# Kernel tuning notes

Measured on AMD Instinct MI355X. Metric: run time of the kernel, lower is better.

The kernel has to match this reference:

```python
import jax, jax.numpy as jnp
import numpy as np

HEIGHT = 8
IN_DIM = 128
OUT_DIM = 8
BATCH = 65536
INT_NODES = 2 ** HEIGHT - 1   # 255
LEAF_NODES = 2 ** HEIGHT      # 256


def _and_weight(height):
    # Fixed +-1 structured routing matrix [leaf, int_nodes] (DGTreg._get_and_layer_params).
    leaf = 2 ** height
    w = np.zeros((leaf, leaf - 1), dtype=np.float32)
    for i in range(height):
        num = 2 ** i
        start = num - 1
        for j in range(start, start + num):
            rb = leaf // num * (j - start)
            rm = rb + leaf // (2 * num)
            re = rb + leaf // num
            w[rb:rm, j] = 1.0
            w[rm:re, j] = -1.0
    return jnp.asarray(w)


def setup_inputs() -> dict:
    key = jax.random.key(0)
    k = jax.random.split(key, 5)
    x = jax.random.normal(k[0], (BATCH, IN_DIM), jnp.float32)
    # orthogonal-ish predicate weight (scaled gaussian), zero bias per module init
    Wp = jax.random.normal(k[1], (INT_NODES, IN_DIM), jnp.float32) / np.sqrt(IN_DIM)
    bp = jnp.zeros((INT_NODES,), jnp.float32)
    Wand = _and_weight(HEIGHT)
    # xavier_uniform for or-layer weights [out_dim, in_dim, leaf]
    lim = np.sqrt(6.0 / (IN_DIM + LEAF_NODES)).astype(np.float32)
    Wor = jax.random.uniform(k[2], (OUT_DIM, IN_DIM, LEAF_NODES), jnp.float32, -lim, lim)
    bor = jax.random.normal(k[3], (OUT_DIM, IN_DIM), jnp.float32) * 0.01
    lim2 = np.sqrt(6.0 / (LEAF_NODES + OUT_DIM)).astype(np.float32)
    action_stds = jax.random.uniform(k[4], (LEAF_NODES, OUT_DIM), jnp.float32, -lim2, lim2)
    return {"x": x, "Wp": Wp, "bp": bp, "Wand": Wand, "Wor": Wor, "bor": bor,
            "action_stds": action_stds}


def reference(x, Wp, bp, Wand, Wor, bor, action_stds):
    sg = jax.lax.stop_gradient
    # predicate layer: [B, int_nodes]
    pred_z = x @ Wp.T + bp
    # ScaleBinarizer1: fac = mean(|z|) per row; binarize to {fac, 0}; straight-through grad
    fac = jnp.mean(jnp.abs(pred_z), axis=-1, keepdims=True)
    binz = jnp.where(pred_z >= 0, fac, 0.0)
    pred_a = pred_z + sg(binz - pred_z)          # forward = binz, grad = identity
    pred_a = 2.0 * pred_a - sg(fac)              # in {+fac, -fac}
    # fixed structured 'and' layer -> softmax over leaves
    and_z = pred_a @ Wand.T                      # [B, leaf]
    and_a = jax.nn.softmax(and_z, axis=-1)
    # Sparser1: keep only max entry per row, straight-through grad
    mx = jnp.max(and_a, axis=-1, keepdims=True)
    sp = jnp.where(and_a >= mx, and_a, 0.0)
    and_a = and_a + sg(sp - and_a)
    # or layers: per-output Linear(leaf->in_dim) then <wt, x>
    wt = jnp.einsum('bl,oil->boi', and_a, Wor) + bor[None]   # [B, out, in]
    out = jnp.einsum('boi,bi->bo', wt, x)                    # [B, out]
    # std head over detached routing weights
    std = jnp.sum(action_stds[None] * sg(and_a)[:, :, None], axis=1)  # [B, out]
    std = jnp.clip(std, -20.0, 2.0)
    return (out, std)
```

## Files before the change

kernel.cpp:

```cpp
#include <hip/hip_runtime.h>

#define BATCH 65536
#define IN_DIM 128
#define INT_NODES 255
#define LEAF 256
#define OUT_DIM 8
#define ROWS_PB 32
#define NBLK (BATCH / ROWS_PB)
#define AMB_TH 4e-3f

typedef float    f4v __attribute__((ext_vector_type(4)));
typedef _Float16 h8v __attribute__((ext_vector_type(8)));

__global__ __launch_bounds__(256) void prep(const float* __restrict__ Wor,
                                            float* __restrict__ Wor_t,
                                            const float* __restrict__ Wp,
                                            _Float16* __restrict__ Bf) {
    if (blockIdx.x < 64) {
        __shared__ float t[64][65];
        const int rt = blockIdx.x >> 2, ct = blockIdx.x & 3;
        const int r0 = rt * 64, c0 = ct * 64;
        const int tx = threadIdx.x & 63, ty = threadIdx.x >> 6;
#pragma unroll
        for (int p = 0; p < 16; ++p) {
            int r = ty + p * 4;
            t[r][tx] = Wor[(size_t)(r0 + r) * 256 + c0 + tx];
        }
        __syncthreads();
#pragma unroll
        for (int p = 0; p < 16; ++p) {
            int r = ty + p * 4;
            Wor_t[(size_t)(c0 + r) * 1024 + r0 + tx] = t[tx][r];
        }
    } else {
        int slot = (blockIdx.x - 64) * 256 + threadIdx.x;
        int j    = slot & 7;
        int lane = (slot >> 3) & 63;
        int ntg  = (slot >> 9) & 15;
        int ks   = slot >> 13;
        int n = ntg * 16 + (lane & 15);
        int k = ks * 32 + (lane >> 4) * 8 + j;
        float v = (n < INT_NODES) ? Wp[n * IN_DIM + k] : 0.f;
        Bf[slot] = (_Float16)v;
    }
}

__global__ __launch_bounds__(256) void dgt_main(
    const float* __restrict__ x, const float* __restrict__ Wp,
    const float* __restrict__ bp, const _Float16* __restrict__ Bfg,
    const float* __restrict__ Wor_t, const float* __restrict__ bor,
    const float* __restrict__ stds,
    float* __restrict__ out, float* __restrict__ stdo) {

    __shared__ unsigned char sgn[LEAF * 8];
    __shared__ float P[64 * 36];
    __shared__ float S[8 * 32];
    __shared__ float H[32 * 68];
    __shared__ float psL[32];
    __shared__ int   leafL[32];

    const int tid  = threadIdx.x;
    const int wave = tid >> 6;
    const int lane = tid & 63;
    const int c = lane & 15;
    const int g = lane >> 4;
    const int rowbase = blockIdx.x * ROWS_PB;

    f4v acc[2][4];
#pragma unroll
    for (int mt = 0; mt < 2; ++mt)
#pragma unroll
        for (int nt = 0; nt < 4; ++nt) acc[mt][nt] = (f4v){0.f, 0.f, 0.f, 0.f};

    const h8v* Bf8 = (const h8v*)Bfg;
    const float* xbase = x + (size_t)rowbase * IN_DIM;
#pragma unroll
    for (int ks = 0; ks < 4; ++ks) {
        h8v ah[2];
#pragma unroll
        for (int mt = 0; mt < 2; ++mt) {
            const float* p = xbase + (size_t)(mt * 16 + c) * IN_DIM + ks * 32 + g * 8;
            float4 v0 = *reinterpret_cast<const float4*>(p);
            float4 v1 = *reinterpret_cast<const float4*>(p + 4);
            h8v a;
            a[0] = (_Float16)v0.x; a[1] = (_Float16)v0.y;
            a[2] = (_Float16)v0.z; a[3] = (_Float16)v0.w;
            a[4] = (_Float16)v1.x; a[5] = (_Float16)v1.y;
            a[6] = (_Float16)v1.z; a[7] = (_Float16)v1.w;
            ah[mt] = a;
        }
#pragma unroll
        for (int nt = 0; nt < 4; ++nt) {
            h8v b = Bf8[(ks * 16 + (wave * 4 + nt)) * 64 + lane];
#pragma unroll
            for (int mt = 0; mt < 2; ++mt)
                acc[mt][nt] = __builtin_amdgcn_mfma_f32_16x16x32_f16(ah[mt], b, acc[mt][nt], 0, 0, 0);
        }
    }

    {
        float pp[2][4];
#pragma unroll
        for (int mt = 0; mt < 2; ++mt)
#pragma unroll
            for (int rr = 0; rr < 4; ++rr) pp[mt][rr] = 0.f;
#pragma unroll
        for (int nt = 0; nt < 4; ++nt) {
            const int n = wave * 64 + nt * 16 + c;
            const float bpv = (n < INT_NODES) ? bp[n] : 0.f;
#pragma unroll
            for (int mt = 0; mt < 2; ++mt) {
                unsigned by = 0;
#pragma unroll
                for (int rr = 0; rr < 4; ++rr) {
                    float v = acc[mt][nt][rr] + bpv;
                    float av = fabsf(v);
                    if (n < INT_NODES) pp[mt][rr] += av;
                    by |= ((v < 0.f ? 1u : 0u) | (av < AMB_TH ? 2u : 0u)) << (2 * rr);
                }
                sgn[n * 8 + mt * 4 + g] = (unsigned char)by;
            }
        }
#pragma unroll
        for (int mt = 0; mt < 2; ++mt)
#pragma unroll
            for (int rr = 0; rr < 4; ++rr)
                P[(wave * 16 + c) * 36 + mt * 16 + g * 4 + rr] = pp[mt][rr];
    }
    __syncthreads();

    {
        const int r = tid & 31, q = tid >> 5;
        float s = 0.f;
#pragma unroll
        for (int cc = 0; cc < 8; ++cc) s += P[(q * 8 + cc) * 36 + r];
        S[q * 32 + r] = s;
    }
    __syncthreads();

    {
        const int r = tid >> 3, kq = tid & 7;
        float asum = 0.f;
#pragma unroll
        for (int j = 0; j < 8; ++j) asum += S[j * 32 + r];
        const float fac = asum * (1.0f / (float)INT_NODES);
        const float e = expf(-2.0f * fac);
        const float qq = 1.0f + e;
        const float q2 = qq * qq, q4 = q2 * q2, q8 = q4 * q4;
        const float ps = 1.0f / q8;

        int node = 0;
#pragma unroll
        for (int d = 0; d < 8; ++d) {
            unsigned by = sgn[node * 8 + (r >> 2)];
            int code = (int)((by >> ((r & 3) * 2)) & 3u);
            int neg;
            if (code & 2) {
                double zd = (double)bp[node];
                const float* wr = Wp + node * IN_DIM;
                const float* xrow = x + (size_t)(rowbase + r) * IN_DIM;
                for (int k = 0; k < IN_DIM; ++k)
                    zd = fma((double)wr[k], (double)xrow[k], zd);
                neg = (zd < 0.0) ? 1 : 0;
            } else {
                neg = code & 1;
            }
            node = 2 * node + 1 + neg;
        }
        const int leaf = node - INT_NODES;
        if (kq == 0) { psL[r] = ps; leafL[r] = leaf; }

        const float* xr = x + (size_t)(rowbase + r) * IN_DIM;
        const float* wl = Wor_t + (size_t)leaf * 1024;
        float hp[8], tp[8];
#pragma unroll
        for (int o = 0; o < 8; ++o) { hp[o] = 0.f; tp[o] = 0.f; }
#pragma unroll
        for (int step = 0; step < 4; ++step) {
            const int off = (step * 8 + kq) * 4;
            float4 xv = *reinterpret_cast<const float4*>(xr + off);
#pragma unroll
            for (int o = 0; o < 8; ++o) {
                float4 wv = *reinterpret_cast<const float4*>(wl + o * IN_DIM + off);
                float4 bv = *reinterpret_cast<const float4*>(bor + o * IN_DIM + off);
                hp[o] = fmaf(wv.x, xv.x, hp[o]); hp[o] = fmaf(wv.y, xv.y, hp[o]);
                hp[o] = fmaf(wv.z, xv.z, hp[o]); hp[o] = fmaf(wv.w, xv.w, hp[o]);
                tp[o] = fmaf(bv.x, xv.x, tp[o]); tp[o] = fmaf(bv.y, xv.y, tp[o]);
                tp[o] = fmaf(bv.z, xv.z, tp[o]); tp[o] = fmaf(bv.w, xv.w, tp[o]);
            }
        }
#pragma unroll
        for (int o = 0; o < 8; ++o)
            H[r * 68 + o * 8 + kq] = ps * hp[o] + tp[o];
    }
    __syncthreads();

    {
        const int r = tid & 31, o = tid >> 5;
        const float* h = &H[r * 68 + o * 8];
        float v = ((h[0] + h[1]) + (h[2] + h[3])) + ((h[4] + h[5]) + (h[6] + h[7]));
        out[(size_t)(rowbase + r) * OUT_DIM + o] = v;
        float sd = psL[r] * stds[leafL[r] * OUT_DIM + o];
        stdo[(size_t)(rowbase + r) * OUT_DIM + o] = fminf(fmaxf(sd, -20.0f), 2.0f);
    }
}

extern "C" void kernel_launch(void* const* d_in, const int* in_sizes, int n_in,
                              void* d_out, int out_size, void* d_ws, size_t ws_size,
                              hipStream_t stream) {
    const float* x    = (const float*)d_in[0];
    const float* Wp   = (const float*)d_in[1];
    const float* bp   = (const float*)d_in[2];
    const float* Wor  = (const float*)d_in[4];
    const float* bor  = (const float*)d_in[5];
    const float* stds = (const float*)d_in[6];
    float* out = (float*)d_out;

    char* ws = (char*)d_ws;
    float* wor_t = (float*)(ws);
    _Float16* Bf = (_Float16*)(ws + (1 << 20));

    prep<<<192, 256, 0, stream>>>(Wor, wor_t, Wp, Bf);
    dgt_main<<<NBLK, 256, 0, stream>>>(x, Wp, bp, Bf, wor_t, bor, stds,
                                       out, out + (size_t)BATCH * OUT_DIM);
}
```

Baseline: 136.5 us.

## Make each wave own 16 rows end-to-end, replacing block barriers with wave-local LDS

Restructures the main kernel so each wavefront independently handles 16 batch rows. It computes all 256 predicate columns via MFMA in two halves, then does routing and the or-layer dot products itself, with per-wave shared-memory scratch. Block-wide __syncthreads are replaced by lgkmcnt waits, and the fac reduction and output stores are reorganized (float2 stores). The aim is to remove cross-wave barriers and the two-stage partial-sum reduction. In exchange each wave now loads all Bf fragments, raising L2 traffic and register pressure. It also relies on intra-wave LDS ordering without explicit barriers.

```diff
diff --git a/kernel.cpp b/kernel.cpp
--- a/kernel.cpp
+++ b/kernel.cpp
@@ -5,12 +5,12 @@
 #define INT_NODES 255
 #define LEAF 256
 #define OUT_DIM 8
-#define ROWS_PB 32
-#define NBLK (BATCH / ROWS_PB)
 #define AMB_TH 4e-3f
 
 typedef float    f4v __attribute__((ext_vector_type(4)));
 typedef _Float16 h8v __attribute__((ext_vector_type(8)));
+
+#define LGKM0() __asm__ volatile("s_waitcnt lgkmcnt(0)" ::: "memory")
 
 __global__ __launch_bounds__(256) void prep(const float* __restrict__ Wor,
                                             float* __restrict__ Wor_t,
@@ -52,34 +52,29 @@
     const float* __restrict__ stds,
     float* __restrict__ out, float* __restrict__ stdo) {
 
-    __shared__ unsigned char sgn[LEAF * 8];
-    __shared__ float P[64 * 36];
-    __shared__ float S[8 * 32];
-    __shared__ float H[32 * 68];
-    __shared__ float psL[32];
-    __shared__ int   leafL[32];
+    __shared__ unsigned char sgnS[4][LEAF * 4];
+    __shared__ float asumS[4][16 * 16];
+    __shared__ float hdS[4][16 * 36];
+    __shared__ float psS[4][16];
+    __shared__ int   lfS[4][16];
 
     const int tid  = threadIdx.x;
     const int wave = tid >> 6;
     const int lane = tid & 63;
     const int c = lane & 15;
     const int g = lane >> 4;
-    const int rowbase = blockIdx.x * ROWS_PB;
-
-    f4v acc[2][4];
-#pragma unroll
-    for (int mt = 0; mt < 2; ++mt)
-#pragma unroll
-        for (int nt = 0; nt < 4; ++nt) acc[mt][nt] = (f4v){0.f, 0.f, 0.f, 0.f};
-
-    const h8v* Bf8 = (const h8v*)Bfg;
-    const float* xbase = x + (size_t)rowbase * IN_DIM;
-#pragma unroll
-    for (int ks = 0; ks < 4; ++ks) {
-        h8v ah[2];
-#pragma unroll
-        for (int mt = 0; mt < 2; ++mt) {
-            const float* p = xbase + (size_t)(mt * 16 + c) * IN_DIM + ks * 32 + g * 8;
+    const int rowbase = blockIdx.x * 64 + wave * 16;
+
+    unsigned char* sgn = sgnS[wave];
+    float* asum = asumS[wave];
+    float* hd = hdS[wave];
+
+    h8v ah[4];
+    {
+        const float* xb = x + (size_t)(rowbase + c) * IN_DIM;
+#pragma unroll
+        for (int ks = 0; ks < 4; ++ks) {
+            const float* p = xb + ks * 32 + g * 8;
             float4 v0 = *reinterpret_cast<const float4*>(p);
             float4 v1 = *reinterpret_cast<const float4*>(p + 4);
             h8v a;
@@ -87,72 +82,60 @@
             a[2] = (_Float16)v0.z; a[3] = (_Float16)v0.w;
             a[4] = (_Float16)v1.x; a[5] = (_Float16)v1.y;
             a[6] = (_Float16)v1.z; a[7] = (_Float16)v1.w;
-            ah[mt] = a;
-        }
-#pragma unroll
-        for (int nt = 0; nt < 4; ++nt) {
-            h8v b = Bf8[(ks * 16 + (wave * 4 + nt)) * 64 + lane];
-#pragma unroll
-            for (int mt = 0; mt < 2; ++mt)
-                acc[mt][nt] = __builtin_amdgcn_mfma_f32_16x16x32_f16(ah[mt], b, acc[mt][nt], 0, 0, 0);
-        }
-    }
-
-    {
-        float pp[2][4];
-#pragma unroll
-        for (int mt = 0; mt < 2; ++mt)
-#pragma unroll
-            for (int rr = 0; rr < 4; ++rr) pp[mt][rr] = 0.f;
-#pragma unroll
-        for (int nt = 0; nt < 4; ++nt) {
-            const int n = wave * 64 + nt * 16 + c;
+            ah[ks] = a;
+        }
+    }
+
+    const h8v* Bf8 = (const h8v*)Bfg;
+    float pp[4] = {0.f, 0.f, 0.f, 0.f};
+#pragma unroll
+    for (int h = 0; h < 2; ++h) {
+        f4v acc[8];
+#pragma unroll
+        for (int nt = 0; nt < 8; ++nt) acc[nt] = (f4v){0.f, 0.f, 0.f, 0.f};
+#pragma unroll
+        for (int ks = 0; ks < 4; ++ks)
+#pragma unroll
+            for (int nt = 0; nt < 8; ++nt) {
+                h8v b = Bf8[(ks * 16 + h * 8 + nt) * 64 + lane];
+                acc[nt] = __builtin_amdgcn_mfma_f32_16x16x32_f16(ah[ks], b, acc[nt], 0, 0, 0);
+            }
+#pragma unroll
+        for (int nt = 0; nt < 8; ++nt) {
+            const int n = h * 128 + nt * 16 + c;
             const float bpv = (n < INT_NODES) ? bp[n] : 0.f;
-#pragma unroll
-            for (int mt = 0; mt < 2; ++mt) {
-                unsigned by = 0;
-#pragma unroll
-                for (int rr = 0; rr < 4; ++rr) {
-                    float v = acc[mt][nt][rr] + bpv;
-                    float av = fabsf(v);
-                    if (n < INT_NODES) pp[mt][rr] += av;
-                    by |= ((v < 0.f ? 1u : 0u) | (av < AMB_TH ? 2u : 0u)) << (2 * rr);
-                }
-                sgn[n * 8 + mt * 4 + g] = (unsigned char)by;
-            }
-        }
-#pragma unroll
-        for (int mt = 0; mt < 2; ++mt)
-#pragma unroll
-            for (int rr = 0; rr < 4; ++rr)
-                P[(wave * 16 + c) * 36 + mt * 16 + g * 4 + rr] = pp[mt][rr];
-    }
-    __syncthreads();
-
-    {
-        const int r = tid & 31, q = tid >> 5;
+            unsigned by = 0;
+#pragma unroll
+            for (int rr = 0; rr < 4; ++rr) {
+                float v = acc[nt][rr] + bpv;
+                float av = fabsf(v);
+                if (n < INT_NODES) pp[rr] += av;
+                by |= ((v < 0.f ? 1u : 0u) | (av < AMB_TH ? 2u : 0u)) << (2 * rr);
+            }
+            sgn[n * 4 + g] = (unsigned char)by;
+        }
+    }
+#pragma unroll
+    for (int rr = 0; rr < 4; ++rr) asum[(g * 4 + rr) * 16 + c] = pp[rr];
+    LGKM0();
+
+    if (lane < 16) {
+        const int r = lane;
         float s = 0.f;
 #pragma unroll
-        for (int cc = 0; cc < 8; ++cc) s += P[(q * 8 + cc) * 36 + r];
-        S[q * 32 + r] = s;
-    }
-    __syncthreads();
-
-    {
-        const int r = tid >> 3, kq = tid & 7;
-        float asum = 0.f;
-#pragma unroll
-        for (int j = 0; j < 8; ++j) asum += S[j * 32 + r];
-        const float fac = asum * (1.0f / (float)INT_NODES);
+        for (int cc = 0; cc < 16; cc += 4) {
+            f4v v = *reinterpret_cast<f4v*>(&asum[r * 16 + cc]);
+            s += (v[0] + v[1]) + (v[2] + v[3]);
+        }
+        const float fac = s * (1.0f / (float)INT_NODES);
         const float e = expf(-2.0f * fac);
-        const float qq = 1.0f + e;
-        const float q2 = qq * qq, q4 = q2 * q2, q8 = q4 * q4;
-        const float ps = 1.0f / q8;
+        const float q = 1.0f + e;
+        const float q2 = q * q, q4 = q2 * q2, q8 = q4 * q4;
 
         int node = 0;
 #pragma unroll
         for (int d = 0; d < 8; ++d) {
-            unsigned by = sgn[node * 8 + (r >> 2)];
+            unsigned by = sgn[node * 4 + (r >> 2)];
             int code = (int)((by >> ((r & 3) * 2)) & 3u);
             int neg;
             if (code & 2) {
@@ -167,17 +150,23 @@
             }
             node = 2 * node + 1 + neg;
         }
-        const int leaf = node - INT_NODES;
-        if (kq == 0) { psL[r] = ps; leafL[r] = leaf; }
-
+        psS[wave][r] = 1.0f / q8;
+        lfS[wave][r] = node - INT_NODES;
+    }
+    LGKM0();
+
+    {
+        const int r = lane >> 2, kq = lane & 3;
+        const int leaf = lfS[wave][r];
+        const float ps = psS[wave][r];
         const float* xr = x + (size_t)(rowbase + r) * IN_DIM;
         const float* wl = Wor_t + (size_t)leaf * 1024;
         float hp[8], tp[8];
 #pragma unroll
         for (int o = 0; o < 8; ++o) { hp[o] = 0.f; tp[o] = 0.f; }
 #pragma unroll
-        for (int step = 0; step < 4; ++step) {
-            const int off = (step * 8 + kq) * 4;
+        for (int step = 0; step < 8; ++step) {
+            const int off = (step * 4 + kq) * 4;
             float4 xv = *reinterpret_cast<const float4*>(xr + off);
 #pragma unroll
             for (int o = 0; o < 8; ++o) {
@@ -191,17 +180,25 @@
         }
 #pragma unroll
         for (int o = 0; o < 8; ++o)
-            H[r * 68 + o * 8 + kq] = ps * hp[o] + tp[o];
-    }
-    __syncthreads();
+            hd[r * 36 + o * 4 + kq] = ps * hp[o] + tp[o];
+    }
+    LGKM0();
 
     {
-        const int r = tid & 31, o = tid >> 5;
-        const float* h = &H[r * 68 + o * 8];
-        float v = ((h[0] + h[1]) + (h[2] + h[3])) + ((h[4] + h[5]) + (h[6] + h[7]));
-        out[(size_t)(rowbase + r) * OUT_DIM + o] = v;
-        float sd = psL[r] * stds[leafL[r] * OUT_DIM + o];
-        stdo[(size_t)(rowbase + r) * OUT_DIM + o] = fminf(fmaxf(sd, -20.0f), 2.0f);
+        const int r = lane >> 2, op = lane & 3, o0 = op * 2;
+        f4v a = *reinterpret_cast<f4v*>(&hd[r * 36 + o0 * 4]);
+        f4v b = *reinterpret_cast<f4v*>(&hd[r * 36 + o0 * 4 + 4]);
+        float2 ov;
+        ov.x = (a[0] + a[1]) + (a[2] + a[3]);
+        ov.y = (b[0] + b[1]) + (b[2] + b[3]);
+        const size_t ob = (size_t)(rowbase + r) * OUT_DIM + o0;
+        *reinterpret_cast<float2*>(out + ob) = ov;
+        const int leaf = lfS[wave][r];
+        const float ps = psS[wave][r];
+        float2 sv;
+        sv.x = fminf(fmaxf(ps * stds[leaf * OUT_DIM + o0],     -20.0f), 2.0f);
+        sv.y = fminf(fmaxf(ps * stds[leaf * OUT_DIM + o0 + 1], -20.0f), 2.0f);
+        *reinterpret_cast<float2*>(stdo + ob) = sv;
     }
 }
 
@@ -221,6 +218,6 @@
     _Float16* Bf = (_Float16*)(ws + (1 << 20));
 
     prep<<<192, 256, 0, stream>>>(Wor, wor_t, Wp, Bf);
-    dgt_main<<<NBLK, 256, 0, stream>>>(x, Wp, bp, Bf, wor_t, bor, stds,
-                                       out, out + (size_t)BATCH * OUT_DIM);
+    dgt_main<<<BATCH / 64, 256, 0, stream>>>(x, Wp, bp, Bf, wor_t, bor, stds,
+                                             out, out + (size_t)BATCH * OUT_DIM);
 }
```

Result: faster. 122.3 us (-10.4%).
